# Performance work log

Hardware: AMD Instinct MI355X
Metric: run time of the kernel (lower is better)

## Reference

```python
import jax, jax.numpy as jnp
import numpy as np

VOCAB = 400000
DIM = 128        # meta['embed_dim']
NBITS = 2        # bits per code
CODEBOOK = 1 << NBITS   # 4 codebook entries
MASK = CODEBOOK - 1
N_WORDS = VOCAB * DIM * NBITS // 32  # 3,200,000 packed int32 words


def setup_inputs() -> dict:
    key = jax.random.key(0)
    k1, k2, k3 = jax.random.split(key, 3)
    input_ids = jax.random.randint(k1, (64, 4096), 0, VOCAB, dtype=jnp.int64)
    # packed bit array: nonnegative int32 words (top bit clear so >> is logical)
    bit_arr = jax.random.randint(k2, (N_WORDS,), 0, 2147483647, dtype=jnp.int32)
    codebook = jax.random.normal(k3, (CODEBOOK,), dtype=jnp.float32)
    return {"input": input_ids, "bit_arr": bit_arr, "codebook": codebook}


def reference(input, bit_arr, codebook):
    flat = input.reshape(-1).astype(jnp.int32)            # [N]
    # code position for (token, dim): p = token*DIM + dim
    pos = flat[:, None] * DIM + jnp.arange(DIM, dtype=jnp.int32)[None, :]  # [N, DIM]
    bitpos = pos * NBITS
    word = bitpos >> 5            # // 32
    shift = bitpos & 31           # % 32
    codes = (bit_arr[word] >> shift) & MASK               # [N, DIM] in [0, 2^NBITS)
    embeds = codebook[codes]                              # [N, DIM] fp32
    return embeds.reshape(input.shape + (DIM,))
```

## Files before the change

### kernel.cpp

```cpp
#include <hip/hip_runtime.h>


#define EMB_DIM 128
#define TOK_PER_WAVE 32
#define WAVES_PER_BLOCK 4
#define TOK_PER_BLOCK (TOK_PER_WAVE * WAVES_PER_BLOCK)
#define BLOCK 256

typedef float vfloat4 __attribute__((ext_vector_type(4)));

__global__ __launch_bounds__(BLOCK) void embed2bit_wave_kernel(
    const int* __restrict__ ids,
    const int* __restrict__ bits,
    const float* __restrict__ cb,
    float* __restrict__ out,
    int n_tokens)
{
    __shared__ int lds_words[TOK_PER_BLOCK * 8];

    const int tid  = threadIdx.x;
    const int w    = tid >> 6;
    const int lane = tid & 63;

    const int tile = blockIdx.x * WAVES_PER_BLOCK + w;
    const int tb   = tile * TOK_PER_WAVE;
    if (tb >= n_tokens) return;
    const int tleft = n_tokens - tb;
    const int ntok  = tleft < TOK_PER_WAVE ? tleft : TOK_PER_WAVE;

    int* lds_w = lds_words + w * (TOK_PER_WAVE * 8);
    const int myTok = lane >> 1;
    if (myTok < ntok) {
        int tok = ids[tb + myTok];
        __builtin_amdgcn_global_load_lds(
            (const __attribute__((address_space(1))) void*)
                (bits + (long long)tok * 8 + (lane & 1) * 4),
            (__attribute__((address_space(3))) void*)(lds_w + lane * 4),
            16, 0, 0);
    }
    asm volatile("s_waitcnt vmcnt(0)" ::: "memory");

    const float c0 = cb[0], c1 = cb[1], c2 = cb[2], c3 = cb[3];
    const long long out_base = (long long)tb * EMB_DIM;
    const int n_items = ntok * 32;

#pragma unroll
    for (int q = 0; q < 16; ++q) {
        int item = q * 64 + lane;
        if (item >= n_items) break;
        int word = lds_w[item >> 2];
        int byte = (word >> ((item & 3) * 8)) & 0xff;

        vfloat4 r;
#pragma unroll
        for (int j = 0; j < 4; ++j) {
            int c    = (byte >> (2 * j)) & 3;
            float lo = (c & 1) ? c1 : c0;
            float hi = (c & 1) ? c3 : c2;
            r[j]     = (c & 2) ? hi : lo;
        }
        *reinterpret_cast<vfloat4*>(out + out_base + (long long)item * 4) = r;
    }
}

extern "C" void kernel_launch(void* const* d_in, const int* in_sizes, int n_in,
                              void* d_out, int out_size, void* d_ws, size_t ws_size,
                              hipStream_t stream) {
    const int*   ids  = (const int*)d_in[0];
    const int*   bits = (const int*)d_in[1];
    const float* cb   = (const float*)d_in[2];
    float*       out  = (float*)d_out;

    int n_tokens = in_sizes[0];
    int grid = (n_tokens + TOK_PER_BLOCK - 1) / TOK_PER_BLOCK;

    embed2bit_wave_kernel<<<grid, BLOCK, 0, stream>>>(ids, bits, cb, out, n_tokens);
}
```

Before: 148.7 us.

## Process two token tiles per wave with overlapped LDS gathers

Each wave now handles two 32-token tiles and issues both global-to-LDS gathers up front. It waits only for the first tile's data before decoding and storing it, so the second tile's gather overlaps that compute. The s_waitcnt counts are hand-tuned, and vmcnt(16) assumes the stores from the first tile are counted in vmcnt. The grid is halved, which lowers parallelism but raises memory-level parallelism per wave.

Measured after the change: 148.9 us. About the same (+0.2%).

```diff
diff --git a/kernel.cpp b/kernel.cpp
--- a/kernel.cpp
+++ b/kernel.cpp
@@ -1,65 +1,103 @@
 #include <hip/hip_runtime.h>
 
 
-#define EMB_DIM 128
-#define TOK_PER_WAVE 32
+#define TOK_PER_TILE 32
+#define TILES_PER_WAVE 2
 #define WAVES_PER_BLOCK 4
+#define BLOCK 256
+#define TOK_PER_WAVE (TOK_PER_TILE * TILES_PER_WAVE)
 #define TOK_PER_BLOCK (TOK_PER_WAVE * WAVES_PER_BLOCK)
-#define BLOCK 256
 
 typedef float vfloat4 __attribute__((ext_vector_type(4)));
 
-__global__ __launch_bounds__(BLOCK) void embed2bit_wave_kernel(
+__global__ __launch_bounds__(BLOCK) void embed2bit_pipe_kernel(
     const int* __restrict__ ids,
     const int* __restrict__ bits,
     const float* __restrict__ cb,
     float* __restrict__ out,
     int n_tokens)
 {
-    __shared__ int lds_words[TOK_PER_BLOCK * 8];
+    __shared__ int lds_words[WAVES_PER_BLOCK * 2 * TOK_PER_TILE * 8];
 
     const int tid  = threadIdx.x;
     const int w    = tid >> 6;
     const int lane = tid & 63;
 
-    const int tile = blockIdx.x * WAVES_PER_BLOCK + w;
-    const int tb   = tile * TOK_PER_WAVE;
-    if (tb >= n_tokens) return;
-    const int tleft = n_tokens - tb;
-    const int ntok  = tleft < TOK_PER_WAVE ? tleft : TOK_PER_WAVE;
+    const long long wid = (long long)blockIdx.x * WAVES_PER_BLOCK + w;
+    const int tb0 = (int)(wid * TOK_PER_WAVE);
+    const int tb1 = tb0 + TOK_PER_TILE;
+    if (tb0 >= n_tokens) return;
 
-    int* lds_w = lds_words + w * (TOK_PER_WAVE * 8);
-    const int myTok = lane >> 1;
-    if (myTok < ntok) {
-        int tok = ids[tb + myTok];
-        __builtin_amdgcn_global_load_lds(
-            (const __attribute__((address_space(1))) void*)
-                (bits + (long long)tok * 8 + (lane & 1) * 4),
-            (__attribute__((address_space(3))) void*)(lds_w + lane * 4),
-            16, 0, 0);
-    }
-    asm volatile("s_waitcnt vmcnt(0)" ::: "memory");
+    const int last = n_tokens - 1;
+    int i0 = tb0 + (lane >> 1); if (i0 > last) i0 = last;
+    int i1 = tb1 + (lane >> 1); if (i1 > last) i1 = last;
+
+    int tok0 = ids[i0];
+    int tok1 = ids[i1];
+
+    int* b0 = lds_words + (w * 2 + 0) * (TOK_PER_TILE * 8);
+    int* b1 = lds_words + (w * 2 + 1) * (TOK_PER_TILE * 8);
+
+    __builtin_amdgcn_global_load_lds(
+        (const __attribute__((address_space(1))) void*)
+            (bits + (long long)tok0 * 8 + (lane & 1) * 4),
+        (__attribute__((address_space(3))) void*)(b0 + lane * 4), 16, 0, 0);
+    __builtin_amdgcn_global_load_lds(
+        (const __attribute__((address_space(1))) void*)
+            (bits + (long long)tok1 * 8 + (lane & 1) * 4),
+        (__attribute__((address_space(3))) void*)(b1 + lane * 4), 16, 0, 0);
 
     const float c0 = cb[0], c1 = cb[1], c2 = cb[2], c3 = cb[3];
-    const long long out_base = (long long)tb * EMB_DIM;
-    const int n_items = ntok * 32;
 
+    asm volatile("s_waitcnt vmcnt(1)" ::: "memory");
+    __builtin_amdgcn_sched_barrier(0);
+    {
+        const long long out_base = (long long)tb0 * 128;
+        const int rem = n_tokens - tb0;
+        const int n_items = (rem >= TOK_PER_TILE ? TOK_PER_TILE : rem) * 32;
 #pragma unroll
-    for (int q = 0; q < 16; ++q) {
-        int item = q * 64 + lane;
-        if (item >= n_items) break;
-        int word = lds_w[item >> 2];
-        int byte = (word >> ((item & 3) * 8)) & 0xff;
+        for (int q = 0; q < 16; ++q) {
+            int item = q * 64 + lane;
+            if (item < n_items) {
+                int word = b0[item >> 2];
+                int byte = (word >> ((item & 3) * 8)) & 0xff;
+                vfloat4 r;
+#pragma unroll
+                for (int j = 0; j < 4; ++j) {
+                    int c    = (byte >> (2 * j)) & 3;
+                    float lo = (c & 1) ? c1 : c0;
+                    float hi = (c & 1) ? c3 : c2;
+                    r[j]     = (c & 2) ? hi : lo;
+                }
+                *reinterpret_cast<vfloat4*>(out + out_base + (long long)item * 4) = r;
+            }
+        }
+    }
 
-        vfloat4 r;
+    asm volatile("s_waitcnt vmcnt(16)" ::: "memory");
+    __builtin_amdgcn_sched_barrier(0);
+    {
+        const long long out_base = (long long)tb1 * 128;
+        const int rem = n_tokens - tb1;
+        const int n_items = (rem <= 0 ? 0
+                             : (rem >= TOK_PER_TILE ? TOK_PER_TILE : rem)) * 32;
 #pragma unroll
-        for (int j = 0; j < 4; ++j) {
-            int c    = (byte >> (2 * j)) & 3;
-            float lo = (c & 1) ? c1 : c0;
-            float hi = (c & 1) ? c3 : c2;
-            r[j]     = (c & 2) ? hi : lo;
+        for (int q = 0; q < 16; ++q) {
+            int item = q * 64 + lane;
+            if (item < n_items) {
+                int word = b1[item >> 2];
+                int byte = (word >> ((item & 3) * 8)) & 0xff;
+                vfloat4 r;
+#pragma unroll
+                for (int j = 0; j < 4; ++j) {
+                    int c    = (byte >> (2 * j)) & 3;
+                    float lo = (c & 1) ? c1 : c0;
+                    float hi = (c & 1) ? c3 : c2;
+                    r[j]     = (c & 2) ? hi : lo;
+                }
+                *reinterpret_cast<vfloat4*>(out + out_base + (long long)item * 4) = r;
+            }
         }
-        *reinterpret_cast<vfloat4*>(out + out_base + (long long)item * 4) = r;
     }
 }
 
@@ -74,5 +112,5 @@
     int n_tokens = in_sizes[0];
     int grid = (n_tokens + TOK_PER_BLOCK - 1) / TOK_PER_BLOCK;
 
-    embed2bit_wave_kernel<<<grid, BLOCK, 0, stream>>>(ids, bits, cb, out, n_tokens);
+    embed2bit_pipe_kernel<<<grid, BLOCK, 0, stream>>>(ids, bits, cb, out, n_tokens);
 }
```
